# Kernel optimization log

Measured on AMD Instinct MI355X. Metric: run time of the kernel, lower is better.

## Reference

```python
import jax, jax.numpy as jnp
import numpy as np

B, P, D, H, A, C = 256, 512, 16, 256, 8, 2
HID = 256
IN_MLP = H + A + 1  # 265


def setup_inputs() -> dict:
    key = jax.random.key(0)
    ks = jax.random.split(key, 12)
    s = 0.05  # small init for recurrent stability
    return {
        "particles": jax.random.normal(ks[0], (B, P, D), jnp.float32),
        "weights": jax.random.uniform(ks[1], (B, P), jnp.float32),
        "actions": jax.random.normal(ks[2], (B, A), jnp.float32),
        "time": jax.random.uniform(ks[3], (B,), jnp.float32) * 100.0,
        "Wi": jax.random.normal(ks[4], (D + 1, 3 * H), jnp.float32) * s,
        "bi": jnp.zeros((3 * H,), jnp.float32),
        "Wh_rz": jax.random.normal(ks[5], (H, 2 * H), jnp.float32) * s,
        "Wh_n": jax.random.normal(ks[6], (H, H), jnp.float32) * s,
        "bn": jnp.zeros((H,), jnp.float32),
        "mlp_W1": jax.random.normal(ks[7], (C, IN_MLP, HID), jnp.float32) * s,
        "mlp_b1": jnp.zeros((C, HID), jnp.float32),
        "mlp_W2": jax.random.normal(ks[8], (C, HID, HID), jnp.float32) * s,
        "mlp_b2": jnp.zeros((C, HID), jnp.float32),
        "mlp_W3": jax.random.normal(ks[9], (C, HID, 1), jnp.float32) * s,
        "mlp_b3": jnp.zeros((C, 1), jnp.float32),
        "num_time_steps": 100,
    }


def reference(particles, weights, actions, time, Wi, bi, Wh_rz, Wh_n, bn,
              mlp_W1, mlp_b1, mlp_W2, mlp_b2, mlp_W3, mlp_b3, num_time_steps):
    # feature_fn = identity; append weights as an extra feature channel
    x = jnp.concatenate([particles, weights[..., None]], axis=-1)  # [B, P, D+1]
    xs = jnp.swapaxes(x, 0, 1)  # [P, B, D+1], scan over particle axis

    def gru_step(h, xt):
        gi = xt @ Wi + bi  # [B, 3H]
        i_r, i_z, i_n = jnp.split(gi, 3, axis=-1)
        hrz = h @ Wh_rz  # [B, 2H], no bias (flax GRUCell hidden r/z dense)
        r = jax.nn.sigmoid(i_r + hrz[:, :H])
        z = jax.nn.sigmoid(i_z + hrz[:, H:])
        n = jnp.tanh(i_n + r * (h @ Wh_n + bn))
        h_new = (1.0 - z) * n + z * h
        return h_new, None

    h0 = jnp.zeros((particles.shape[0], H), particles.dtype)
    enc, _ = jax.lax.scan(gru_step, h0, xs)  # last hidden == take(outputs, -1, axis=-2)

    norm_time = time / num_time_steps
    hidden = jnp.concatenate([enc, actions, norm_time[..., None]], axis=-1)  # [B, IN_MLP]

    # n_critics MLPs evaluated batched over critic axis c
    h1 = jax.nn.relu(jnp.einsum('bi,cio->bco', hidden, mlp_W1) + mlp_b1)
    h2 = jax.nn.relu(jnp.einsum('bci,cio->bco', h1, mlp_W2) + mlp_b2)
    q = jnp.einsum('bci,cio->bco', h2, mlp_W3) + mlp_b3  # [B, C, 1]
    return q[..., 0]  # [B, C]
```

## Files before the change

kernel.cpp:

```cpp
#include <hip/hip_runtime.h>
#include <hip/hip_fp16.h>

typedef _Float16 h2v __attribute__((ext_vector_type(2)));
typedef unsigned int u32;
typedef unsigned short u16;

#define NB 256
#define NP 512
#define NH 256
#define NCOL 768

#define OFF_WH 0
#define LEN_WH 98304
#define OFF_WI (OFF_WH + LEN_WH)
#define LEN_WI 6912
#define OFF_W1 (OFF_WI + LEN_WI)
#define LEN_W1 68096
#define OFF_W2 (OFF_W1 + LEN_W1)
#define LEN_W2 65536
#define OFF_W3 (OFF_W2 + LEN_W2)
#define LEN_W3 256
#define WS_DWORDS (OFF_W3 + LEN_W3)

__device__ __forceinline__ u32 pack2(float lo, float hi) {
    h2v v; v.x = (_Float16)lo; v.y = (_Float16)hi;
    return __builtin_bit_cast(u32, v);
}

__device__ __forceinline__ float fdot2(u32 a, u32 b, float c) {
#if __has_builtin(__builtin_amdgcn_fdot2)
    return __builtin_amdgcn_fdot2(__builtin_bit_cast(h2v, a),
                                  __builtin_bit_cast(h2v, b), c, false);
#else
    h2v x = __builtin_bit_cast(h2v, a), y = __builtin_bit_cast(h2v, b);
    return c + (float)x.x * (float)y.x + (float)x.y * (float)y.y;
#endif
}

__global__ __launch_bounds__(256) void pack_kernel(
    const float* __restrict__ Wi, const float* __restrict__ Whrz,
    const float* __restrict__ Whn, const float* __restrict__ W1,
    const float* __restrict__ W2, const float* __restrict__ W3,
    u32* __restrict__ ws)
{
    for (int F = blockIdx.x * 256 + threadIdx.x; F < WS_DWORDS; F += gridDim.x * 256) {
        u32 val;
        if (F < OFF_WI) {
            int l = F & 63; int t = F >> 6;
            int i = t % 192; int wid = t / 192;
            int c = i >> 5, kk = i & 31;
            int kw = wid & 3, cg = wid >> 2;
            int k = 64 * kw + 2 * kk;
            int col = 384 * cg + 64 * c + l;
            float lo, hi;
            if (col < 512) { lo = Whrz[k * 512 + col]; hi = Whrz[(k + 1) * 512 + col]; }
            else { lo = Whn[k * 256 + (col - 512)]; hi = Whn[(k + 1) * 256 + (col - 512)]; }
            val = pack2(lo, hi);
        } else if (F < OFF_W1) {
            int j = F - OFF_WI; int kk = j / NCOL; int col = j % NCOL;
            int k = 2 * kk;
            float lo = Wi[k * NCOL + col];
            float hi = (k + 1 < 17) ? Wi[(k + 1) * NCOL + col] : 0.f;
            val = pack2(lo, hi);
        } else if (F < OFF_W2) {
            int j = F - OFF_W1; int c = j / (133 * 256); int r = j % (133 * 256);
            int kk = r >> 8; int o = r & 255;
            int k = 2 * kk;
            float lo = W1[(c * 265 + k) * 256 + o];
            float hi = (k + 1 < 265) ? W1[(c * 265 + k + 1) * 256 + o] : 0.f;
            val = pack2(lo, hi);
        } else if (F < OFF_W3) {
            int j = F - OFF_W2; int c = j >> 15; int r = j & 32767;
            int kk = r >> 8; int o = r & 255;
            float lo = W2[(c * 256 + 2 * kk) * 256 + o];
            float hi = W2[(c * 256 + 2 * kk + 1) * 256 + o];
            val = pack2(lo, hi);
        } else {
            int j = F - OFF_W3; int c = j >> 7; int jj = j & 127;
            float lo = W3[c * 256 + 2 * jj];
            float hi = W3[c * 256 + 2 * jj + 1];
            val = pack2(lo, hi);
        }
        ws[F] = val;
    }
}

__global__ __launch_bounds__(512, 2) void qnet_kernel(
    const float* __restrict__ particles, const float* __restrict__ pweights,
    const float* __restrict__ actions, const float* __restrict__ timev,
    const float* __restrict__ bi, const float* __restrict__ bn,
    const float* __restrict__ b1, const float* __restrict__ b2,
    const float* __restrict__ b3, const int* __restrict__ nts,
    const u32* __restrict__ ws, float* __restrict__ out)
{
    __shared__ __align__(16) u32 sWi[LEN_WI];
    __shared__ __align__(16) u32 sX[NP * 9];
    __shared__ __align__(16) float sPart[4 * NCOL];
    __shared__ __align__(16) u32 sH2[NH / 2];
    __shared__ __align__(16) float sHf[NH];
    __shared__ __align__(16) float sMisc[16];

    u32* sHid = sWi;
    u16* sL1 = (u16*)sX;
    u16* sL2 = (u16*)sPart;

    const int b = blockIdx.x;
    const int tid = threadIdx.x;
    const int lane = tid & 63;
    const int wid = tid >> 6;
    const int kw = wid & 3;
    const int cg = wid >> 2;

    u32 wreg[192];
    {
        const u32* gp = ws + OFF_WH + (wid * 192) * 64 + lane;
        #pragma unroll
        for (int i = 0; i < 192; ++i) wreg[i] = gp[i * 64];
    }
    for (int j = tid; j < LEN_WI; j += 512) sWi[j] = ws[OFF_WI + j];
    {
        const float4* pr = (const float4*)(particles + (long)b * NP * 16);
        for (int j = tid; j < NP * 4; j += 512) {
            float4 v = pr[j];
            int p = j >> 2, d4 = j & 3;
            sX[p * 9 + d4 * 2]     = pack2(v.x, v.y);
            sX[p * 9 + d4 * 2 + 1] = pack2(v.z, v.w);
        }
        const float* wr = pweights + (long)b * NP;
        for (int p = tid; p < NP; p += 512) sX[p * 9 + 8] = pack2(wr[p], 0.f);
    }
    if (tid < NH / 2) sH2[tid] = 0u;
    if (tid < 8) sMisc[tid] = actions[b * 8 + tid];
    if (tid == 8) sMisc[8] = timev[b] / (float)nts[0];

    float hreg = 0.f, bir = 0.f, biz = 0.f, binn = 0.f, bnn = 0.f;
    if (tid < NH) {
        bir = bi[tid]; biz = bi[NH + tid]; binn = bi[2 * NH + tid]; bnn = bn[tid];
    }
    __syncthreads();

    const int colbase = cg * 384 + lane;
    #pragma unroll 1
    for (int p = 0; p < NP; ++p) {
        float acc[6] = {0.f, 0.f, 0.f, 0.f, 0.f, 0.f};
        const uint4* h4 = ((const uint4*)sH2) + kw * 8;
        #pragma unroll
        for (int q = 0; q < 8; ++q) {
            uint4 hv = h4[q];
            u32 hp[4] = {hv.x, hv.y, hv.z, hv.w};
            #pragma unroll
            for (int j = 0; j < 4; ++j) {
                #pragma unroll
                for (int c = 0; c < 6; ++c)
                    acc[c] = fdot2(wreg[c * 32 + q * 4 + j], hp[j], acc[c]);
            }
        }
        #pragma unroll
        for (int c = 0; c < 6; ++c)
            sPart[kw * NCOL + colbase + 64 * c] = acc[c];

        float xr = 0.f, xz = 0.f, xn = 0.f;
        if (tid < NH) {
            xr = bir; xz = biz; xn = binn;
            const u32* xp = &sX[p * 9];
            #pragma unroll
            for (int kk = 0; kk < 9; ++kk) {
                u32 xv = xp[kk];
                xr = fdot2(sWi[kk * NCOL + tid], xv, xr);
                xz = fdot2(sWi[kk * NCOL + NH + tid], xv, xz);
                xn = fdot2(sWi[kk * NCOL + 2 * NH + tid], xv, xn);
            }
        }
        __syncthreads();
        if (tid < NH) {
            float sr = sPart[tid] + sPart[NCOL + tid] + sPart[2 * NCOL + tid] + sPart[3 * NCOL + tid];
            float sz = sPart[NH + tid] + sPart[NCOL + NH + tid] + sPart[2 * NCOL + NH + tid] + sPart[3 * NCOL + NH + tid];
            float sn = sPart[2 * NH + tid] + sPart[NCOL + 2 * NH + tid] + sPart[2 * NCOL + 2 * NH + tid] + sPart[3 * NCOL + 2 * NH + tid];
            float r = 1.f / (1.f + __expf(-(sr + xr)));
            float z = 1.f / (1.f + __expf(-(sz + xz)));
            float targ = xn + r * (sn + bnn);
            float e2 = __expf(2.f * targ);
            float n = 1.f - 2.f / (e2 + 1.f);
            hreg = (1.f - z) * n + z * hreg;
            _Float16 hh = (_Float16)hreg;
            ((u16*)sH2)[tid] = __builtin_bit_cast(u16, hh);
        }
        __syncthreads();
    }

    if (tid < NH) sHf[tid] = hreg;
    __syncthreads();
    if (tid < 128) sHid[tid] = pack2(sHf[2 * tid], sHf[2 * tid + 1]);
    else if (tid < 132) { int i = tid - 128; sHid[tid] = pack2(sMisc[2 * i], sMisc[2 * i + 1]); }
    else if (tid == 132) sHid[132] = pack2(sMisc[8], 0.f);
    __syncthreads();
    {
        int c = tid >> 8, o = tid & 255;
        float acc = b1[c * 256 + o];
        const u32* wp = ws + OFF_W1 + c * 133 * 256 + o;
        #pragma unroll 4
        for (int kk = 0; kk < 133; ++kk) acc = fdot2(wp[kk * 256], sHid[kk], acc);
        acc = fmaxf(acc, 0.f);
        _Float16 a16 = (_Float16)acc;
        sL1[tid] = __builtin_bit_cast(u16, a16);
    }
    __syncthreads();
    {
        int c = tid >> 8, o = tid & 255;
        float acc = b2[c * 256 + o];
        const u32* wp = ws + OFF_W2 + c * 128 * 256 + o;
        const u32* hp = (const u32*)sL1 + c * 128;
        #pragma unroll 4
        for (int kk = 0; kk < 128; ++kk) acc = fdot2(wp[kk * 256], hp[kk], acc);
        acc = fmaxf(acc, 0.f);
        _Float16 a16 = (_Float16)acc;
        sL2[tid] = __builtin_bit_cast(u16, a16);
    }
    __syncthreads();
    if (tid < 128) {
        int c = tid >> 6, l = tid & 63;
        const u32* wp = ws + OFF_W3 + c * 128;
        const u32* hp = (const u32*)sL2 + c * 128;
        float acc = fdot2(wp[l], hp[l], 0.f);
        acc = fdot2(wp[64 + l], hp[64 + l], acc);
        #pragma unroll
        for (int off = 32; off > 0; off >>= 1) acc += __shfl_down(acc, off);
        if (l == 0) out[b * 2 + c] = acc + b3[c];
    }
}

extern "C" void kernel_launch(void* const* d_in, const int* in_sizes, int n_in,
                              void* d_out, int out_size, void* d_ws, size_t ws_size,
                              hipStream_t stream) {
    const float* particles = (const float*)d_in[0];
    const float* pweights  = (const float*)d_in[1];
    const float* actions   = (const float*)d_in[2];
    const float* timev     = (const float*)d_in[3];
    const float* Wi        = (const float*)d_in[4];
    const float* bi        = (const float*)d_in[5];
    const float* Whrz      = (const float*)d_in[6];
    const float* Whn       = (const float*)d_in[7];
    const float* bn        = (const float*)d_in[8];
    const float* W1        = (const float*)d_in[9];
    const float* b1        = (const float*)d_in[10];
    const float* W2        = (const float*)d_in[11];
    const float* b2        = (const float*)d_in[12];
    const float* W3        = (const float*)d_in[13];
    const float* b3        = (const float*)d_in[14];
    const int*   nts       = (const int*)d_in[15];
    u32* ws = (u32*)d_ws;
    float* outp = (float*)d_out;

    pack_kernel<<<WS_DWORDS / 256, 256, 0, stream>>>(Wi, Whrz, Whn, W1, W2, W3, ws);
    qnet_kernel<<<NB, 512, 0, stream>>>(particles, pweights, actions, timev,
                                        bi, bn, b1, b2, b3, nts, ws, outp);
}
```

Before: 700.5 us.

## Halve block to 256 threads, hold full recurrent weights and Wi in registers

Shrinks the GRU block from 512 to 256 threads, so each wave keeps 384 packed Wh dwords plus 27 Wi dwords in registers and computes 12 output columns instead of 6. The Wi projection now reads registers and vectorized particle rows instead of shared memory, and all threads take part in the gate update. Fewer waves means less barrier and partial-sum traffic per step, but register pressure is very high (over 400 VGPRs, which needs AGPRs or risks spilling) and there are fewer waves to hide latency.

Result: slower. 1.070 ms (+52.8%).

```diff
diff --git a/kernel.cpp b/kernel.cpp
--- a/kernel.cpp
+++ b/kernel.cpp
@@ -47,17 +47,18 @@
         u32 val;
         if (F < OFF_WI) {
             int l = F & 63; int t = F >> 6;
-            int i = t % 192; int wid = t / 192;
-            int c = i >> 5, kk = i & 31;
-            int kw = wid & 3, cg = wid >> 2;
-            int k = 64 * kw + 2 * kk;
-            int col = 384 * cg + 64 * c + l;
+            int kk2 = t & 31; int t2 = t >> 5;
+            int j = t2 % 12; int w = t2 / 12;
+            int k = 64 * w + 2 * kk2;
+            int col = 64 * j + l;
             float lo, hi;
             if (col < 512) { lo = Whrz[k * 512 + col]; hi = Whrz[(k + 1) * 512 + col]; }
             else { lo = Whn[k * 256 + (col - 512)]; hi = Whn[(k + 1) * 256 + (col - 512)]; }
             val = pack2(lo, hi);
         } else if (F < OFF_W1) {
-            int j = F - OFF_WI; int kk = j / NCOL; int col = j % NCOL;
+            int j = F - OFF_WI; int g = j & 255; int i = j >> 8;
+            int g3 = i / 9; int kk = i % 9;
+            int col = 256 * g3 + g;
             int k = 2 * kk;
             float lo = Wi[k * NCOL + col];
             float hi = (k + 1 < 17) ? Wi[(k + 1) * NCOL + col] : 0.f;
@@ -85,7 +86,7 @@
     }
 }
 
-__global__ __launch_bounds__(512, 2) void qnet_kernel(
+__global__ __launch_bounds__(256, 1) void qnet_kernel(
     const float* __restrict__ particles, const float* __restrict__ pweights,
     const float* __restrict__ actions, const float* __restrict__ timev,
     const float* __restrict__ bi, const float* __restrict__ bn,
@@ -93,89 +94,99 @@
     const float* __restrict__ b3, const int* __restrict__ nts,
     const u32* __restrict__ ws, float* __restrict__ out)
 {
-    __shared__ __align__(16) u32 sWi[LEN_WI];
-    __shared__ __align__(16) u32 sX[NP * 9];
+    __shared__ __align__(16) u32 sX[NP * 12];
     __shared__ __align__(16) float sPart[4 * NCOL];
     __shared__ __align__(16) u32 sH2[NH / 2];
     __shared__ __align__(16) float sHf[NH];
     __shared__ __align__(16) float sMisc[16];
-
-    u32* sHid = sWi;
-    u16* sL1 = (u16*)sX;
-    u16* sL2 = (u16*)sPart;
+    __shared__ __align__(16) u32 sHid[136];
+    __shared__ __align__(16) u16 sL1[512];
+    __shared__ __align__(16) u16 sL2[512];
 
     const int b = blockIdx.x;
     const int tid = threadIdx.x;
-    const int lane = tid & 63;
-    const int wid = tid >> 6;
-    const int kw = wid & 3;
-    const int cg = wid >> 2;
-
-    u32 wreg[192];
-    {
-        const u32* gp = ws + OFF_WH + (wid * 192) * 64 + lane;
-        #pragma unroll
-        for (int i = 0; i < 192; ++i) wreg[i] = gp[i * 64];
-    }
-    for (int j = tid; j < LEN_WI; j += 512) sWi[j] = ws[OFF_WI + j];
+    const int l = tid & 63;
+    const int w = tid >> 6;
+
+    u32 wregs[384];
+    {
+        const u32* gp = ws + OFF_WH + (w * 384) * 64 + l;
+        #pragma unroll
+        for (int i = 0; i < 384; ++i) wregs[i] = gp[i * 64];
+    }
+    u32 wiR[27];
+    #pragma unroll
+    for (int i = 0; i < 27; ++i) wiR[i] = ws[OFF_WI + i * 256 + tid];
+    #pragma unroll
+    for (int i = 0; i < 384; ++i) asm volatile("" : "+v"(wregs[i]));
+    #pragma unroll
+    for (int i = 0; i < 27; ++i) asm volatile("" : "+v"(wiR[i]));
+
     {
         const float4* pr = (const float4*)(particles + (long)b * NP * 16);
-        for (int j = tid; j < NP * 4; j += 512) {
-            float4 v = pr[j];
-            int p = j >> 2, d4 = j & 3;
-            sX[p * 9 + d4 * 2]     = pack2(v.x, v.y);
-            sX[p * 9 + d4 * 2 + 1] = pack2(v.z, v.w);
+        #pragma unroll
+        for (int it = 0; it < 8; ++it) {
+            int f = tid + 256 * it;
+            float4 v = pr[f];
+            int p = f >> 2, d4 = f & 3;
+            sX[p * 12 + d4 * 2]     = pack2(v.x, v.y);
+            sX[p * 12 + d4 * 2 + 1] = pack2(v.z, v.w);
         }
         const float* wr = pweights + (long)b * NP;
-        for (int p = tid; p < NP; p += 512) sX[p * 9 + 8] = pack2(wr[p], 0.f);
+        sX[tid * 12 + 8] = pack2(wr[tid], 0.f);
+        sX[(tid + 256) * 12 + 8] = pack2(wr[tid + 256], 0.f);
     }
     if (tid < NH / 2) sH2[tid] = 0u;
     if (tid < 8) sMisc[tid] = actions[b * 8 + tid];
     if (tid == 8) sMisc[8] = timev[b] / (float)nts[0];
 
-    float hreg = 0.f, bir = 0.f, biz = 0.f, binn = 0.f, bnn = 0.f;
-    if (tid < NH) {
-        bir = bi[tid]; biz = bi[NH + tid]; binn = bi[2 * NH + tid]; bnn = bn[tid];
-    }
-    __syncthreads();
-
-    const int colbase = cg * 384 + lane;
+    const float bir = bi[tid], biz = bi[NH + tid], binn = bi[2 * NH + tid], bnn = bn[tid];
+    float hreg = 0.f;
+    __syncthreads();
+
     #pragma unroll 1
     for (int p = 0; p < NP; ++p) {
-        float acc[6] = {0.f, 0.f, 0.f, 0.f, 0.f, 0.f};
-        const uint4* h4 = ((const uint4*)sH2) + kw * 8;
-        #pragma unroll
-        for (int q = 0; q < 8; ++q) {
-            uint4 hv = h4[q];
-            u32 hp[4] = {hv.x, hv.y, hv.z, hv.w};
-            #pragma unroll
-            for (int j = 0; j < 4; ++j) {
-                #pragma unroll
-                for (int c = 0; c < 6; ++c)
-                    acc[c] = fdot2(wreg[c * 32 + q * 4 + j], hp[j], acc[c]);
-            }
-        }
-        #pragma unroll
-        for (int c = 0; c < 6; ++c)
-            sPart[kw * NCOL + colbase + 64 * c] = acc[c];
-
-        float xr = 0.f, xz = 0.f, xn = 0.f;
-        if (tid < NH) {
-            xr = bir; xz = biz; xn = binn;
-            const u32* xp = &sX[p * 9];
+        float xr = bir, xz = biz, xn = binn;
+        {
+            uint4 xa = *(const uint4*)&sX[p * 12];
+            uint4 xb = *(const uint4*)&sX[p * 12 + 4];
+            u32 x8 = sX[p * 12 + 8];
+            u32 xv[9] = {xa.x, xa.y, xa.z, xa.w, xb.x, xb.y, xb.z, xb.w, x8};
             #pragma unroll
             for (int kk = 0; kk < 9; ++kk) {
-                u32 xv = xp[kk];
-                xr = fdot2(sWi[kk * NCOL + tid], xv, xr);
-                xz = fdot2(sWi[kk * NCOL + NH + tid], xv, xz);
-                xn = fdot2(sWi[kk * NCOL + 2 * NH + tid], xv, xn);
+                xr = fdot2(wiR[kk],      xv[kk], xr);
+                xz = fdot2(wiR[9 + kk],  xv[kk], xz);
+                xn = fdot2(wiR[18 + kk], xv[kk], xn);
             }
         }
+        float acc[12];
+        #pragma unroll
+        for (int j = 0; j < 12; ++j) acc[j] = 0.f;
+        {
+            const uint4* h4 = ((const uint4*)sH2) + w * 8;
+            #pragma unroll
+            for (int q = 0; q < 8; ++q) {
+                uint4 hv = h4[q];
+                u32 hp[4] = {hv.x, hv.y, hv.z, hv.w};
+                #pragma unroll
+                for (int m = 0; m < 4; ++m) {
+                    #pragma unroll
+                    for (int j = 0; j < 12; ++j)
+                        acc[j] = fdot2(wregs[j * 32 + q * 4 + m], hp[m], acc[j]);
+                }
+            }
+        }
+        #pragma unroll
+        for (int j = 0; j < 12; ++j)
+            sPart[w * NCOL + j * 64 + l] = acc[j];
         __syncthreads();
-        if (tid < NH) {
-            float sr = sPart[tid] + sPart[NCOL + tid] + sPart[2 * NCOL + tid] + sPart[3 * NCOL + tid];
-            float sz = sPart[NH + tid] + sPart[NCOL + NH + tid] + sPart[2 * NCOL + NH + tid] + sPart[3 * NCOL + NH + tid];
-            float sn = sPart[2 * NH + tid] + sPart[NCOL + 2 * NH + tid] + sPart[2 * NCOL + 2 * NH + tid] + sPart[3 * NCOL + 2 * NH + tid];
+        {
+            float sr = sPart[tid]            + sPart[NCOL + tid]
+                     + sPart[2 * NCOL + tid] + sPart[3 * NCOL + tid];
+            float sz = sPart[NH + tid]            + sPart[NCOL + NH + tid]
+                     + sPart[2 * NCOL + NH + tid] + sPart[3 * NCOL + NH + tid];
+            float sn = sPart[2 * NH + tid]            + sPart[NCOL + 2 * NH + tid]
+                     + sPart[2 * NCOL + 2 * NH + tid] + sPart[3 * NCOL + 2 * NH + tid];
             float r = 1.f / (1.f + __expf(-(sr + xr)));
             float z = 1.f / (1.f + __expf(-(sz + xz)));
             float targ = xn + r * (sn + bnn);
@@ -188,44 +199,48 @@
         __syncthreads();
     }
 
-    if (tid < NH) sHf[tid] = hreg;
+    sHf[tid] = hreg;
     __syncthreads();
     if (tid < 128) sHid[tid] = pack2(sHf[2 * tid], sHf[2 * tid + 1]);
     else if (tid < 132) { int i = tid - 128; sHid[tid] = pack2(sMisc[2 * i], sMisc[2 * i + 1]); }
     else if (tid == 132) sHid[132] = pack2(sMisc[8], 0.f);
     __syncthreads();
     {
-        int c = tid >> 8, o = tid & 255;
-        float acc = b1[c * 256 + o];
-        const u32* wp = ws + OFF_W1 + c * 133 * 256 + o;
-        #pragma unroll 4
-        for (int kk = 0; kk < 133; ++kk) acc = fdot2(wp[kk * 256], sHid[kk], acc);
-        acc = fmaxf(acc, 0.f);
-        _Float16 a16 = (_Float16)acc;
-        sL1[tid] = __builtin_bit_cast(u16, a16);
-    }
-    __syncthreads();
-    {
-        int c = tid >> 8, o = tid & 255;
-        float acc = b2[c * 256 + o];
-        const u32* wp = ws + OFF_W2 + c * 128 * 256 + o;
-        const u32* hp = (const u32*)sL1 + c * 128;
-        #pragma unroll 4
-        for (int kk = 0; kk < 128; ++kk) acc = fdot2(wp[kk * 256], hp[kk], acc);
-        acc = fmaxf(acc, 0.f);
-        _Float16 a16 = (_Float16)acc;
-        sL2[tid] = __builtin_bit_cast(u16, a16);
+        #pragma unroll
+        for (int c = 0; c < 2; ++c) {
+            float acc = b1[c * 256 + tid];
+            const u32* wp = ws + OFF_W1 + c * 133 * 256 + tid;
+            #pragma unroll 4
+            for (int kk = 0; kk < 133; ++kk) acc = fdot2(wp[kk * 256], sHid[kk], acc);
+            acc = fmaxf(acc, 0.f);
+            _Float16 a16 = (_Float16)acc;
+            sL1[c * 256 + tid] = __builtin_bit_cast(u16, a16);
+        }
+    }
+    __syncthreads();
+    {
+        #pragma unroll
+        for (int c = 0; c < 2; ++c) {
+            float acc = b2[c * 256 + tid];
+            const u32* wp = ws + OFF_W2 + c * 128 * 256 + tid;
+            const u32* hp = (const u32*)sL1 + c * 128;
+            #pragma unroll 4
+            for (int kk = 0; kk < 128; ++kk) acc = fdot2(wp[kk * 256], hp[kk], acc);
+            acc = fmaxf(acc, 0.f);
+            _Float16 a16 = (_Float16)acc;
+            sL2[c * 256 + tid] = __builtin_bit_cast(u16, a16);
+        }
     }
     __syncthreads();
     if (tid < 128) {
-        int c = tid >> 6, l = tid & 63;
+        int c = tid >> 6, ll = tid & 63;
         const u32* wp = ws + OFF_W3 + c * 128;
         const u32* hp = (const u32*)sL2 + c * 128;
-        float acc = fdot2(wp[l], hp[l], 0.f);
-        acc = fdot2(wp[64 + l], hp[64 + l], acc);
+        float acc = fdot2(wp[ll], hp[ll], 0.f);
+        acc = fdot2(wp[64 + ll], hp[64 + ll], acc);
         #pragma unroll
         for (int off = 32; off > 0; off >>= 1) acc += __shfl_down(acc, off);
-        if (l == 0) out[b * 2 + c] = acc + b3[c];
+        if (ll == 0) out[b * 2 + c] = acc + b3[c];
     }
 }
 
@@ -252,6 +267,6 @@
     float* outp = (float*)d_out;
 
     pack_kernel<<<WS_DWORDS / 256, 256, 0, stream>>>(Wi, Whrz, Whn, W1, W2, W3, ws);
-    qnet_kernel<<<NB, 512, 0, stream>>>(particles, pweights, actions, timev,
+    qnet_kernel<<<NB, 256, 0, stream>>>(particles, pweights, actions, timev,
                                         bi, bn, b1, b2, b3, nts, ws, outp);
 }
```
